# Kernel tuning notes

Measured on AMD Instinct MI355X. Metric: run time of the kernel, lower is better.

Reference implementation:

```python
import jax, jax.numpy as jnp
import numpy as np
from jax import lax

N = 16384
M = 16384
C = 64
NUM_CORR = 2048
EPS = 1e-08


def setup_inputs() -> dict:
    key = jax.random.key(0)
    k1, k2, k3, k4 = jax.random.split(key, 4)
    src_points = jax.random.normal(k1, (N, 3), dtype=jnp.float32)
    tgt_points = jax.random.normal(k2, (M, 3), dtype=jnp.float32)
    # features are L2-normalized descriptors in the original pipeline
    src_feats = jax.random.normal(k3, (N, C), dtype=jnp.float32)
    tgt_feats = jax.random.normal(k4, (M, C), dtype=jnp.float32)
    src_feats = src_feats / jnp.linalg.norm(src_feats, axis=-1, keepdims=True)
    tgt_feats = tgt_feats / jnp.linalg.norm(tgt_feats, axis=-1, keepdims=True)
    return {"src_points": src_points, "tgt_points": tgt_points,
            "src_feats": src_feats, "tgt_feats": tgt_feats}


def _match_one_side(q_points, s_points, q_feats, s_feats):
    # brute-force feature kNN (k=2) by squared euclidean distance
    # dist2[n,m] = ||q_n||^2 - 2 q_n.s_m + ||s_m||^2
    dist2 = (jnp.sum(q_feats * q_feats, axis=-1, keepdims=True)
             - 2.0 * (q_feats @ s_feats.T)
             + jnp.sum(s_feats * s_feats, axis=-1)[None, :])  # [N, M]
    _, knn_indices = lax.top_k(-dist2, 2)  # [N, 2]
    knn_feats = s_feats[knn_indices]  # [N, 2, C]
    knn_similarities = 1.0 - jnp.einsum('nkc,nc->nk', knn_feats, q_feats)  # [N, 2]
    # Lowe's ratio test weight
    weights = 1.0 - knn_similarities[:, 0] / (knn_similarities[:, 1] + EPS)  # [N]
    _, q_corr_indices = lax.top_k(weights, NUM_CORR)  # [K]
    s_corr_indices = knn_indices[q_corr_indices, 0]  # [K]
    return (q_points[q_corr_indices], s_points[s_corr_indices],
            q_feats[q_corr_indices], s_feats[s_corr_indices],
            weights[q_corr_indices])


def reference(src_points, tgt_points, src_feats, tgt_feats):
    (s1_pts, t1_pts, s1_feats, t1_feats, w1) = _match_one_side(
        src_points, tgt_points, src_feats, tgt_feats)
    (t2_pts, s2_pts, t2_feats, s2_feats, w2) = _match_one_side(
        tgt_points, src_points, tgt_feats, src_feats)
    src_corr_points = jnp.concatenate([s1_pts, s2_pts], axis=0)
    tgt_corr_points = jnp.concatenate([t1_pts, t2_pts], axis=0)
    src_corr_feats = jnp.concatenate([s1_feats, s2_feats], axis=0)
    tgt_corr_feats = jnp.concatenate([t1_feats, t2_feats], axis=0)
    corr_weights = jnp.concatenate([w1, w2], axis=0)
    return (src_corr_points, tgt_corr_points, src_corr_feats,
            tgt_corr_feats, corr_weights)
```

## Files before the change

### kernel.cpp

```cpp
#include <hip/hip_runtime.h>

#define NPTS 16384
#define CF 64
#define KCORR 2048
#define TCAND 64

__device__ __forceinline__ float dot_avx2(const float* __restrict__ a,
                                          const float* __restrict__ b) {
#pragma clang fp contract(off)
    float v0 = 0.f, v1 = 0.f, v2 = 0.f, v3 = 0.f;
    float v4 = 0.f, v5 = 0.f, v6 = 0.f, v7 = 0.f;
    #pragma unroll
    for (int i = 0; i < CF; i += 8) {
        v0 = fmaf(a[i + 0], b[i + 0], v0);
        v1 = fmaf(a[i + 1], b[i + 1], v1);
        v2 = fmaf(a[i + 2], b[i + 2], v2);
        v3 = fmaf(a[i + 3], b[i + 3], v3);
        v4 = fmaf(a[i + 4], b[i + 4], v4);
        v5 = fmaf(a[i + 5], b[i + 5], v5);
        v6 = fmaf(a[i + 6], b[i + 6], v6);
        v7 = fmaf(a[i + 7], b[i + 7], v7);
    }
    float u0 = v0 + v4, u1 = v1 + v5, u2 = v2 + v6, u3 = v3 + v7;
    float t0 = u0 + u2, t1 = u1 + u3;
    return t0 + t1;
}

__device__ __forceinline__ float row_sumsq(const float* __restrict__ x) {
#pragma clang fp contract(off)
    float r[8];
    #pragma unroll
    for (int j = 0; j < 8; ++j) r[j] = x[j] * x[j];
    #pragma unroll
    for (int i = 8; i < 64; i += 8) {
        #pragma unroll
        for (int j = 0; j < 8; ++j) { float p = x[i + j] * x[i + j]; r[j] = r[j] + p; }
    }
    return ((r[0] + r[1]) + (r[2] + r[3])) + ((r[4] + r[5]) + (r[6] + r[7]));
}

__global__ __launch_bounds__(256) void prep_kernel(
    const float* __restrict__ src_feats, const float* __restrict__ tgt_feats,
    float* __restrict__ qq_src, float* __restrict__ qq_tgt)
{
    int t = blockIdx.x * 256 + threadIdx.x;
    if (t >= 2 * NPTS) return;
    const float* f = (t < NPTS) ? src_feats : tgt_feats;
    float*      qq = (t < NPTS) ? qq_src    : qq_tgt;
    int n = (t < NPTS) ? t : t - NPTS;
    float x[CF];
    #pragma unroll
    for (int c = 0; c < CF; c += 4) {
        float4 v = *(const float4*)(f + (size_t)n * CF + c);
        x[c] = v.x; x[c+1] = v.y; x[c+2] = v.z; x[c+3] = v.w;
    }
    qq[n] = row_sumsq(x);
}

__global__ __launch_bounds__(256, 2) void top2_kernel(
    const float* __restrict__ src_feats, const float* __restrict__ tgt_feats,
    const float* __restrict__ qq_src, const float* __restrict__ qq_tgt,
    float* __restrict__ pd0, float* __restrict__ pd1,
    int* __restrict__ pi0, int* __restrict__ pi1,
    int nch, int chsz)
{
    const int side = blockIdx.z;
    const int ch   = blockIdx.y;
    const int tid  = threadIdx.x;
    const int n    = blockIdx.x * 256 + tid;

    const float* qf = (side == 0) ? src_feats : tgt_feats;
    const float* sf = (side == 0) ? tgt_feats : src_feats;
    const float* qq = (side == 0) ? qq_src    : qq_tgt;
    const float* ss = (side == 0) ? qq_tgt    : qq_src;

    __shared__ float sd[TCAND][CF];
    __shared__ float sss[TCAND];

    float4 qv[16];
    {
        const float4* q4 = (const float4*)(qf + (size_t)n * CF);
        #pragma unroll
        for (int g = 0; g < 16; ++g) qv[g] = q4[g];
    }
    const float qqn = qq[n];

    float d0 = 3.4e38f, d1 = 3.4e38f;
    int i0 = 0, i1 = 0;

    const int m0 = ch * chsz;
    float* sflat = &sd[0][0];
    for (int t0 = 0; t0 < chsz; t0 += TCAND) {
        __syncthreads();
        const float4* g4 = (const float4*)(sf + (size_t)(m0 + t0) * CF);
        #pragma unroll
        for (int k = 0; k < 4; ++k) {
            int idx = k * 256 + tid;
            float4 v = g4[idx];
            sflat[idx*4+0] = v.x; sflat[idx*4+1] = v.y;
            sflat[idx*4+2] = v.z; sflat[idx*4+3] = v.w;
        }
        if (tid < TCAND) sss[tid] = ss[m0 + t0 + tid];
        __syncthreads();

        for (int mm = 0; mm < TCAND; ++mm) {
            const float4* s4 = (const float4*)sd[mm];
            float acc = 0.0f;
            #pragma unroll
            for (int g = 0; g < 16; ++g) {
                float4 sv = s4[g];
                acc = fmaf(qv[g].x, sv.x, acc);
                acc = fmaf(qv[g].y, sv.y, acc);
                acc = fmaf(qv[g].z, sv.z, acc);
                acc = fmaf(qv[g].w, sv.w, acc);
            }
            float d2;
            {
#pragma clang fp contract(off)
                float twod = 2.0f * acc;
                float t1v  = qqn - twod;
                d2 = t1v + sss[mm];
            }
            int m = m0 + t0 + mm;
            if (d2 < d1) {
                if (d2 < d0) { d1 = d0; i1 = i0; d0 = d2; i0 = m; }
                else         { d1 = d2; i1 = m; }
            }
        }
    }
    size_t slot = ((size_t)side * nch + ch) * NPTS + n;
    pd0[slot] = d0; pd1[slot] = d1;
    pi0[slot] = i0; pi1[slot] = i1;
}

__global__ __launch_bounds__(256) void merge_kernel(
    const float* __restrict__ src_feats, const float* __restrict__ tgt_feats,
    const float* __restrict__ pd0, const float* __restrict__ pd1,
    const int* __restrict__ pi0, const int* __restrict__ pi1,
    int nch,
    float* __restrict__ wgt, int* __restrict__ bidx)
{
    int t = blockIdx.x * blockDim.x + threadIdx.x;
    if (t >= 2 * NPTS) return;
    int side = t >> 14, n = t & (NPTS - 1);

    float d0 = 3.4e38f, d1 = 3.4e38f;
    int i0 = 0, i1 = 0;
    for (int ch = 0; ch < nch; ++ch) {
        size_t slot = ((size_t)side * nch + ch) * NPTS + n;
        float cd0 = pd0[slot], cd1 = pd1[slot];
        int   ci0 = pi0[slot], ci1 = pi1[slot];
        if (cd0 < d1) {
            if (cd0 < d0) { d1 = d0; i1 = i0; d0 = cd0; i0 = ci0; }
            else          { d1 = cd0; i1 = ci0; }
        }
        if (cd1 < d1) {
            if (cd1 < d0) { d1 = d0; i1 = i0; d0 = cd1; i0 = ci1; }
            else          { d1 = cd1; i1 = ci1; }
        }
    }
    if (i0 < 0) i0 = 0;
    if (i1 < 0) i1 = 0;

    const float* qf = (side == 0) ? src_feats : tgt_feats;
    const float* sf = (side == 0) ? tgt_feats : src_feats;

    float q[CF];
    #pragma unroll
    for (int c = 0; c < CF; c += 4) {
        float4 v = *(const float4*)(qf + (size_t)n * CF + c);
        q[c] = v.x; q[c+1] = v.y; q[c+2] = v.z; q[c+3] = v.w;
    }

    float dotA = dot_avx2(sf + (size_t)i0 * CF, q);
    float dotB = dot_avx2(sf + (size_t)i1 * CF, q);

    float w;
    {
#pragma clang fp contract(off)
        float sim0 = 1.0f - dotA;
        float sim1 = 1.0f - dotB;
        float den  = sim1 + 1e-8f;
        w = 1.0f - sim0 / den;
    }
    wgt[t]  = w;
    bidx[t] = i0;
}

__global__ __launch_bounds__(256) void rank_gather_kernel(
    const float* __restrict__ wgt, const int* __restrict__ bidx,
    const float* __restrict__ src_points, const float* __restrict__ tgt_points,
    const float* __restrict__ src_feats,  const float* __restrict__ tgt_feats,
    float* __restrict__ out)
{
    const int side = blockIdx.y;
    const int n = blockIdx.x * 256 + threadIdx.x;
    const float* w = wgt + (size_t)side * NPTS;
    const float wn = w[n];

    __shared__ float tile[4096];
    int cnt = 0;
    for (int t0 = 0; t0 < NPTS; t0 += 4096) {
        __syncthreads();
        for (int j = threadIdx.x; j < 4096; j += 256) tile[j] = w[t0 + j];
        __syncthreads();
        #pragma unroll 8
        for (int j = 0; j < 4096; ++j) {
            float wj = tile[j];
            int jj = t0 + j;
            cnt += (wj > wn) || (wj == wn && jj < n);
        }
    }

    if (cnt < KCORR) {
        int r = side * KCORR + cnt;
        int sidx = bidx[(size_t)side * NPTS + n];
        if (sidx < 0) sidx = 0;
        int src_row = (side == 0) ? n : sidx;
        int tgt_row = (side == 0) ? sidx : n;

        float* out_srcP = out;
        float* out_tgtP = out + 2 * KCORR * 3;
        float* out_srcF = out + 4 * KCORR * 3;
        float* out_tgtF = out_srcF + 2 * KCORR * CF;
        float* out_w    = out_tgtF + 2 * KCORR * CF;

        #pragma unroll
        for (int k = 0; k < 3; ++k) {
            out_srcP[(size_t)r * 3 + k] = src_points[(size_t)src_row * 3 + k];
            out_tgtP[(size_t)r * 3 + k] = tgt_points[(size_t)tgt_row * 3 + k];
        }
        const float4* sfr = (const float4*)(src_feats + (size_t)src_row * CF);
        const float4* tfr = (const float4*)(tgt_feats + (size_t)tgt_row * CF);
        float4* so = (float4*)(out_srcF + (size_t)r * CF);
        float4* to = (float4*)(out_tgtF + (size_t)r * CF);
        #pragma unroll
        for (int c = 0; c < CF / 4; ++c) { so[c] = sfr[c]; to[c] = tfr[c]; }
        out_w[r] = wn;
    }
}

extern "C" void kernel_launch(void* const* d_in, const int* in_sizes, int n_in,
                              void* d_out, int out_size, void* d_ws, size_t ws_size,
                              hipStream_t stream)
{
    const float* src_points = (const float*)d_in[0];
    const float* tgt_points = (const float*)d_in[1];
    const float* src_feats  = (const float*)d_in[2];
    const float* tgt_feats  = (const float*)d_in[3];
    float* out = (float*)d_out;
    (void)in_sizes; (void)n_in; (void)out_size;

    auto rup = [](size_t b) { return (b + 255) & ~(size_t)255; };
    size_t base = rup(sizeof(float) * NPTS) * 2
                + rup(sizeof(float) * 2 * NPTS)
                + rup(sizeof(int) * 2 * NPTS);
    size_t per_chunk = rup(sizeof(float) * 2 * NPTS) * 2
                     + rup(sizeof(int) * 2 * NPTS) * 2;
    int nch = 16;
    while (nch > 1 && base + (size_t)nch * per_chunk > ws_size) nch >>= 1;
    int chsz = NPTS / nch;
    size_t nslots = (size_t)2 * nch * NPTS;

    char* ws = (char*)d_ws;
    size_t off = 0;
    auto alloc = [&](size_t bytes) -> void* {
        void* p = ws + off;
        off += (bytes + 255) & ~(size_t)255;
        return p;
    };
    float* qq_src = (float*)alloc(sizeof(float) * NPTS);
    float* qq_tgt = (float*)alloc(sizeof(float) * NPTS);
    float* wgt    = (float*)alloc(sizeof(float) * 2 * NPTS);
    int*   bidx   = (int*)alloc(sizeof(int) * 2 * NPTS);
    float* pd0    = (float*)alloc(sizeof(float) * nslots);
    float* pd1    = (float*)alloc(sizeof(float) * nslots);
    int*   pi0    = (int*)alloc(sizeof(int) * nslots);
    int*   pi1    = (int*)alloc(sizeof(int) * nslots);

    prep_kernel<<<(2 * NPTS + 255) / 256, 256, 0, stream>>>(
        src_feats, tgt_feats, qq_src, qq_tgt);

    top2_kernel<<<dim3(NPTS / 256, nch, 2), 256, 0, stream>>>(
        src_feats, tgt_feats, qq_src, qq_tgt,
        pd0, pd1, pi0, pi1, nch, chsz);

    merge_kernel<<<(2 * NPTS + 255) / 256, 256, 0, stream>>>(
        src_feats, tgt_feats, pd0, pd1, pi0, pi1, nch, wgt, bidx);

    rank_gather_kernel<<<dim3(NPTS / 256, 2), 256, 0, stream>>>(
        wgt, bidx, src_points, tgt_points, src_feats, tgt_feats, out);
}
```

Baseline: 1.475 ms.

## Stream candidate features through scalar loads instead of LDS tiles

Replaces the shared-memory tiling of candidate feature rows with per-candidate s_load_dwordx16 scalar loads into SGPRs. FMAs then take scalar operands directly, which removes LDS traffic and the block barriers. The cost is a full s_waitcnt on every candidate with no prefetch, so scalar memory latency sits on the critical path. The minimum-occupancy launch bound is also dropped.

```diff
diff --git a/kernel.cpp b/kernel.cpp
--- a/kernel.cpp
+++ b/kernel.cpp
@@ -3,7 +3,8 @@
 #define NPTS 16384
 #define CF 64
 #define KCORR 2048
-#define TCAND 64
+
+typedef float f32x16 __attribute__((ext_vector_type(16)));
 
 __device__ __forceinline__ float dot_avx2(const float* __restrict__ a,
                                           const float* __restrict__ b) {
@@ -57,7 +58,7 @@
     qq[n] = row_sumsq(x);
 }
 
-__global__ __launch_bounds__(256, 2) void top2_kernel(
+__global__ __launch_bounds__(256) void top2_kernel(
     const float* __restrict__ src_feats, const float* __restrict__ tgt_feats,
     const float* __restrict__ qq_src, const float* __restrict__ qq_tgt,
     float* __restrict__ pd0, float* __restrict__ pd1,
@@ -74,9 +75,6 @@
     const float* qq = (side == 0) ? qq_src    : qq_tgt;
     const float* ss = (side == 0) ? qq_tgt    : qq_src;
 
-    __shared__ float sd[TCAND][CF];
-    __shared__ float sss[TCAND];
-
     float4 qv[16];
     {
         const float4* q4 = (const float4*)(qf + (size_t)n * CF);
@@ -88,44 +86,52 @@
     float d0 = 3.4e38f, d1 = 3.4e38f;
     int i0 = 0, i1 = 0;
 
-    const int m0 = ch * chsz;
-    float* sflat = &sd[0][0];
-    for (int t0 = 0; t0 < chsz; t0 += TCAND) {
-        __syncthreads();
-        const float4* g4 = (const float4*)(sf + (size_t)(m0 + t0) * CF);
-        #pragma unroll
-        for (int k = 0; k < 4; ++k) {
-            int idx = k * 256 + tid;
-            float4 v = g4[idx];
-            sflat[idx*4+0] = v.x; sflat[idx*4+1] = v.y;
-            sflat[idx*4+2] = v.z; sflat[idx*4+3] = v.w;
-        }
-        if (tid < TCAND) sss[tid] = ss[m0 + t0 + tid];
-        __syncthreads();
-
-        for (int mm = 0; mm < TCAND; ++mm) {
-            const float4* s4 = (const float4*)sd[mm];
-            float acc = 0.0f;
-            #pragma unroll
-            for (int g = 0; g < 16; ++g) {
-                float4 sv = s4[g];
-                acc = fmaf(qv[g].x, sv.x, acc);
-                acc = fmaf(qv[g].y, sv.y, acc);
-                acc = fmaf(qv[g].z, sv.z, acc);
-                acc = fmaf(qv[g].w, sv.w, acc);
-            }
-            float d2;
-            {
-#pragma clang fp contract(off)
-                float twod = 2.0f * acc;
-                float t1v  = qqn - twod;
-                d2 = t1v + sss[mm];
-            }
-            int m = m0 + t0 + mm;
-            if (d2 < d1) {
-                if (d2 < d0) { d1 = d0; i1 = i0; d0 = d2; i0 = m; }
-                else         { d1 = d2; i1 = m; }
-            }
+    const int m0 = ch * chsz, m1 = m0 + chsz;
+    for (int m = m0; m < m1; ++m) {
+        const float* sp = sf + (size_t)m * CF;
+        f32x16 b0, b1, b2, b3;
+        asm("s_load_dwordx16 %0, %4, 0x0\n\t"
+            "s_load_dwordx16 %1, %4, 0x40\n\t"
+            "s_load_dwordx16 %2, %4, 0x80\n\t"
+            "s_load_dwordx16 %3, %4, 0xc0\n\t"
+            "s_waitcnt lgkmcnt(0)"
+            : "=&s"(b0), "=&s"(b1), "=&s"(b2), "=&s"(b3)
+            : "s"(sp));
+
+        float acc = 0.0f;
+        #define ACC16(B, G)                                            \
+            acc = fmaf(qv[(G)+0].x, B[ 0], acc);                       \
+            acc = fmaf(qv[(G)+0].y, B[ 1], acc);                       \
+            acc = fmaf(qv[(G)+0].z, B[ 2], acc);                       \
+            acc = fmaf(qv[(G)+0].w, B[ 3], acc);                       \
+            acc = fmaf(qv[(G)+1].x, B[ 4], acc);                       \
+            acc = fmaf(qv[(G)+1].y, B[ 5], acc);                       \
+            acc = fmaf(qv[(G)+1].z, B[ 6], acc);                       \
+            acc = fmaf(qv[(G)+1].w, B[ 7], acc);                       \
+            acc = fmaf(qv[(G)+2].x, B[ 8], acc);                       \
+            acc = fmaf(qv[(G)+2].y, B[ 9], acc);                       \
+            acc = fmaf(qv[(G)+2].z, B[10], acc);                       \
+            acc = fmaf(qv[(G)+2].w, B[11], acc);                       \
+            acc = fmaf(qv[(G)+3].x, B[12], acc);                       \
+            acc = fmaf(qv[(G)+3].y, B[13], acc);                       \
+            acc = fmaf(qv[(G)+3].z, B[14], acc);                       \
+            acc = fmaf(qv[(G)+3].w, B[15], acc);
+        ACC16(b0, 0)
+        ACC16(b1, 4)
+        ACC16(b2, 8)
+        ACC16(b3, 12)
+        #undef ACC16
+
+        float d2;
+        {
+#pragma clang fp contract(off)
+            float twod = 2.0f * acc;
+            float t1v  = qqn - twod;
+            d2 = t1v + ss[m];
+        }
+        if (d2 < d1) {
+            if (d2 < d0) { d1 = d0; i1 = i0; d0 = d2; i0 = m; }
+            else         { d1 = d2; i1 = m; }
         }
     }
     size_t slot = ((size_t)side * nch + ch) * NPTS + n;
```

New measurement: 1.553 ms. 1.05x slower.
